# Kernel tuning notes

Measured on AMD Instinct MI355X. Metric: run time of the kernel, lower is better.

The kernel has to match this reference:

```python
import jax, jax.numpy as jnp
import numpy as np

N, D = 16384, 256

def setup_inputs() -> dict:
    key = jax.random.key(0)
    k1, k2 = jax.random.split(key)
    image_features = jax.random.normal(k1, (N, D), dtype=jnp.float32)
    text_features = jax.random.normal(k2, (N, D), dtype=jnp.float32)
    logit_scale = jnp.float32(14.285714)  # exp(log(1/0.07)), typical CLIP temperature
    targets = jnp.arange(N, dtype=jnp.int64)
    return {"image_features": image_features, "text_features": text_features,
            "logit_scale": logit_scale, "targets": targets}

def _cross_entropy(logits, targets):
    # mean over rows of -log_softmax(logits)[i, targets[i]]
    logp = jax.nn.log_softmax(logits, axis=-1)
    return -jnp.mean(jnp.take_along_axis(logp, targets[:, None], axis=-1))

def reference(image_features, text_features, logit_scale, targets):
    logits = logit_scale * (image_features @ text_features.T)  # [N, N]
    image_loss = _cross_entropy(logits, targets)
    text_loss = _cross_entropy(logits.T, targets)
    return (image_loss + text_loss) / 2.0
```

## Files before the change

### kernel.cpp

```cpp
#include <hip/hip_runtime.h>

#define N_ 16384
#define D_ 256
#define LOG2E 1.4426950408889634f
#define HEXP2(x) __builtin_amdgcn_exp2f(x)

typedef __attribute__((ext_vector_type(8))) short short8;
typedef __attribute__((ext_vector_type(16))) float floatx16;

typedef __attribute__((address_space(1))) const unsigned int gu32_t;
typedef __attribute__((address_space(3))) unsigned int lu32_t;

__device__ __forceinline__ void async16(const void* g, void* l) {
  __builtin_amdgcn_global_load_lds((gu32_t*)g, (lu32_t*)l, 16, 0, 0);
}

__device__ __forceinline__ unsigned short f2bf(float x) {
  unsigned int u = __float_as_uint(x);
  u += 0x7fffu + ((u >> 16) & 1u);
  return (unsigned short)(u >> 16);
}

__global__ void prep_pack(const float* __restrict__ img, const float* __restrict__ txt,
                          const float* __restrict__ ls, short* __restrict__ PA,
                          short* __restrict__ PB, float* __restrict__ accv) {
  int t = blockIdx.x * 256 + threadIdx.x;
  int row = t >> 5, kq = t & 31;
  int G = row >> 5, m = row & 31, ks = kq >> 1, h = kq & 1;
  int uidx = (G * 16 + ks) * 64 + h * 32 + m;
  float s2 = ls[0] * LOG2E;
  const float4* sa = (const float4*)(img + (size_t)row * D_ + kq * 8);
  const float4* sb = (const float4*)(txt + (size_t)row * D_ + kq * 8);
  float4 a0 = sa[0], a1 = sa[1];
  float4 b0 = sb[0], b1 = sb[1];
  short8 oa, ob;
  oa[0] = (short)f2bf(a0.x * s2); oa[1] = (short)f2bf(a0.y * s2);
  oa[2] = (short)f2bf(a0.z * s2); oa[3] = (short)f2bf(a0.w * s2);
  oa[4] = (short)f2bf(a1.x * s2); oa[5] = (short)f2bf(a1.y * s2);
  oa[6] = (short)f2bf(a1.z * s2); oa[7] = (short)f2bf(a1.w * s2);
  ob[0] = (short)f2bf(b0.x); ob[1] = (short)f2bf(b0.y);
  ob[2] = (short)f2bf(b0.z); ob[3] = (short)f2bf(b0.w);
  ob[4] = (short)f2bf(b1.x); ob[5] = (short)f2bf(b1.y);
  ob[6] = (short)f2bf(b1.z); ob[7] = (short)f2bf(b1.w);
  ((short8*)PA)[uidx] = oa;
  ((short8*)PB)[uidx] = ob;
  if (t == 0) accv[0] = 0.0f;
}

__global__ void diag_kernel(const float* __restrict__ img, const float* __restrict__ txt,
                            const float* __restrict__ ls, float* __restrict__ diag2) {
  int row = blockIdx.x * 4 + (threadIdx.x >> 6);
  int lane = threadIdx.x & 63;
  float4 a = ((const float4*)(img + (size_t)row * D_))[lane];
  float4 b = ((const float4*)(txt + (size_t)row * D_))[lane];
  float s = a.x * b.x + a.y * b.y + a.z * b.z + a.w * b.w;
  #pragma unroll
  for (int off = 1; off < 64; off <<= 1) s += __shfl_xor(s, off);
  if (lane == 0) diag2[row] = s * ls[0] * LOG2E;
}

__global__ __launch_bounds__(256, 2)
void gemm_stats(const short* __restrict__ PA, const short* __restrict__ PB,
                float2* __restrict__ pR, float2* __restrict__ pC) {
  __shared__ __align__(16) char smem[73728];
  float* rowbuf  = (float*)(smem + 32768);
  float2* colbuf = (float2*)(smem + 71680);

  const int tid = threadIdx.x, lane = tid & 63, wv = tid >> 6;
  const int wr = wv >> 1, wc = wv & 1;
  const int m = lane & 31, h = lane >> 5;
  const int stripe = blockIdx.x, by = blockIdx.y;

  short8 areg[2][16];
  #pragma unroll
  for (int g = 0; g < 2; ++g)
    #pragma unroll
    for (int ks = 0; ks < 16; ++ks)
      areg[g][ks] = *(const short8*)(PA +
          ((size_t)((stripe * 4 + wr * 2 + g) * 16 + ks)) * 512 + lane * 8);
  asm volatile("s_waitcnt vmcnt(0)" ::: "memory");

  floatx16 acc[2][2];

  auto issue = [&](int jj2, int c2, int bufsel) {
    const short* base = PB + ((size_t)((by * 64 + jj2 * 4) * 16) + c2 * 4 + wv) * 512 + lane * 8;
    char* dst = smem + bufsel * 16384 + wv * 1024;
    #pragma unroll
    for (int ct = 0; ct < 4; ++ct)
      async16(base + (size_t)ct * 8192, dst + ct * 4096);
  };
  auto compute = [&](int c, int bufsel) {
    char* base = smem + bufsel * 16384 + lane * 16;
    #pragma unroll
    for (int ksl = 0; ksl < 4; ++ksl) {
      short8 b0 = *(const short8*)(base + ((wc * 2 + 0) * 4 + ksl) * 1024);
      short8 b1 = *(const short8*)(base + ((wc * 2 + 1) * 4 + ksl) * 1024);
      int ks = c * 4 + ksl;
      acc[0][0] = __builtin_amdgcn_mfma_f32_32x32x16_bf16(areg[0][ks], b0, acc[0][0], 0, 0, 0);
      acc[1][0] = __builtin_amdgcn_mfma_f32_32x32x16_bf16(areg[1][ks], b0, acc[1][0], 0, 0, 0);
      acc[0][1] = __builtin_amdgcn_mfma_f32_32x32x16_bf16(areg[0][ks], b1, acc[0][1], 0, 0, 0);
      acc[1][1] = __builtin_amdgcn_mfma_f32_32x32x16_bf16(areg[1][ks], b1, acc[1][1], 0, 0, 0);
    }
  };

  issue(0, 0, 0);
  issue(0, 1, 1);

  float Mr = -3.0e38f, Sr = 0.f;

  for (int jj = 0; jj < 16; ++jj) {
    #pragma unroll
    for (int rt = 0; rt < 2; ++rt)
      #pragma unroll
      for (int ctl = 0; ctl < 2; ++ctl)
        #pragma unroll
        for (int r = 0; r < 16; ++r) acc[rt][ctl][r] = 0.f;

    #pragma unroll
    for (int c = 0; c < 4; ++c) {
      if (jj == 15 && c == 3) { asm volatile("s_waitcnt vmcnt(0)" ::: "memory"); }
      else                    { asm volatile("s_waitcnt vmcnt(4)" ::: "memory"); }
      __builtin_amdgcn_s_barrier();
      asm volatile("" ::: "memory");
      compute(c, c & 1);
      asm volatile("" ::: "memory");
      __builtin_amdgcn_s_barrier();
      asm volatile("" ::: "memory");
      int nc = c + 2;
      int jj2 = jj + (nc >> 2);
      if (jj2 < 16) issue(jj2, nc & 3, nc & 1);
    }

    float v = -3.0e38f;
    #pragma unroll
    for (int rt = 0; rt < 2; ++rt)
      #pragma unroll
      for (int ctl = 0; ctl < 2; ++ctl)
        #pragma unroll
        for (int r = 0; r < 16; ++r) v = fmaxf(v, acc[rt][ctl][r]);
    #pragma unroll
    for (int off = 1; off < 64; off <<= 1) v = fmaxf(v, __shfl_xor(v, off));
    float msub = v - 96.f;

    #pragma unroll
    for (int rt = 0; rt < 2; ++rt)
      #pragma unroll
      for (int ctl = 0; ctl < 2; ++ctl)
        #pragma unroll
        for (int r = 0; r < 16; ++r) acc[rt][ctl][r] = HEXP2(acc[rt][ctl][r] - msub);

    #pragma unroll
    for (int ctl = 0; ctl < 2; ++ctl) {
      float cp = 0.f;
      #pragma unroll
      for (int r = 0; r < 16; ++r) cp += acc[0][ctl][r] + acc[1][ctl][r];
      cp += __shfl_xor(cp, 32);
      if (h == 0) colbuf[wr * 128 + wc * 64 + ctl * 32 + m] = make_float2(msub, cp);
    }

    #pragma unroll
    for (int rt = 0; rt < 2; ++rt)
      #pragma unroll
      for (int rq = 0; rq < 4; ++rq) {
        float4 rp;
        rp.x = acc[rt][0][rq * 4 + 0] + acc[rt][1][rq * 4 + 0];
        rp.y = acc[rt][0][rq * 4 + 1] + acc[rt][1][rq * 4 + 1];
        rp.z = acc[rt][0][rq * 4 + 2] + acc[rt][1][rq * 4 + 2];
        rp.w = acc[rt][0][rq * 4 + 3] + acc[rt][1][rq * 4 + 3];
        *(float4*)&rowbuf[(wr * 64 + wc * 32 + m) * 76 + rt * 32 + rq * 8 + h * 4] = rp;
      }
    asm volatile("s_waitcnt lgkmcnt(0)" ::: "memory");
    __builtin_amdgcn_s_barrier();
    asm volatile("" ::: "memory");

    {
      float s = 0.f;
      #pragma unroll
      for (int k = 0; k < 32; ++k)
        s += rowbuf[(wr * 64 + h * 32 + k) * 76 + wc * 32 + m];
      s += __shfl_xor(s, 32);
      if (s > 0.f) {
        if (msub > Mr) { Sr = Sr * HEXP2(Mr - msub) + s; Mr = msub; }
        else           { Sr += s * HEXP2(msub - Mr); }
      }
    }
    if (tid < 128) {
      float2 c0 = colbuf[tid], c1 = colbuf[128 + tid];
      float M = -3.0e38f, L = 0.f;
      if (c0.y > 0.f) { M = c0.x; L = c0.y; }
      if (c1.y > 0.f) {
        if (c1.x > M) { L = L * HEXP2(M - c1.x) + c1.y; M = c1.x; }
        else          { L += c1.y * HEXP2(c1.x - M); }
      }
      pC[(size_t)stripe * N_ + by * 2048 + jj * 128 + tid] = make_float2(M, L);
    }
    asm volatile("s_waitcnt lgkmcnt(0)" ::: "memory");
    __builtin_amdgcn_s_barrier();
    asm volatile("" ::: "memory");
  }

  if (h == 0)
    pR[(size_t)by * N_ + stripe * 128 + wr * 64 + wc * 32 + m] = make_float2(Mr, Sr);
}

__global__ void merge_kernel(const float2* __restrict__ pR, const float2* __restrict__ pC,
                             const float* __restrict__ diag2, float* __restrict__ accv) {
  int idx = blockIdx.x * 256 + threadIdx.x;
  float M = -3.0e38f, L = 0.f;
  int i;
  if (idx < N_) {
    i = idx;
    #pragma unroll
    for (int g = 0; g < 8; ++g) {
      float2 w = pR[(size_t)g * N_ + i];
      if (w.y > 0.f) {
        if (w.x > M) { L = L * exp2f(M - w.x) + w.y; M = w.x; }
        else         { L += w.y * exp2f(w.x - M); }
      }
    }
  } else {
    i = idx - N_;
    for (int s = 0; s < 128; ++s) {
      float2 w = pC[(size_t)s * N_ + i];
      if (w.y > 0.f) {
        if (w.x > M) { L = L * exp2f(M - w.x) + w.y; M = w.x; }
        else         { L += w.y * exp2f(w.x - M); }
      }
    }
  }
  float val = (M + log2f(fmaxf(L, 1e-45f))) - diag2[i];

  __shared__ float red[256];
  red[threadIdx.x] = val;
  __syncthreads();
  #pragma unroll
  for (int s = 128; s > 0; s >>= 1) {
    if (threadIdx.x < s) red[threadIdx.x] += red[threadIdx.x + s];
    __syncthreads();
  }
  if (threadIdx.x == 0) atomicAdd(accv, red[0]);
}

__global__ void finalize_kernel(const float* __restrict__ accv, float* __restrict__ out) {
  out[0] = accv[0] * (0.69314718055994531f / 32768.0f);
}

extern "C" void kernel_launch(void* const* d_in, const int* in_sizes, int n_in,
                              void* d_out, int out_size, void* d_ws, size_t ws_size,
                              hipStream_t stream) {
  const float* img = (const float*)d_in[0];
  const float* txt = (const float*)d_in[1];
  const float* ls  = (const float*)d_in[2];
  float* out = (float*)d_out;

  char* ws = (char*)d_ws;
  short* PA    = (short*)(ws);
  short* PB    = (short*)(ws + 8388608);
  float* diag2 = (float*)(ws + 16777216);
  float* accv  = (float*)(ws + 16842752);
  float2* pR   = (float2*)(ws + 16843008);
  float2* pC   = (float2*)(ws + 17891584);

  hipLaunchKernelGGL(prep_pack, dim3(2048), dim3(256), 0, stream, img, txt, ls, PA, PB, accv);
  hipLaunchKernelGGL(diag_kernel, dim3(N_ / 4), dim3(256), 0, stream, img, txt, ls, diag2);
  hipLaunchKernelGGL(gemm_stats, dim3(128, 8), dim3(256), 0, stream, PA, PB, pR, pC);
  hipLaunchKernelGGL(merge_kernel, dim3(2 * N_ / 256), dim3(256), 0, stream, pR, pC, diag2, accv);
  hipLaunchKernelGGL(finalize_kernel, dim3(1), dim3(1), 0, stream, accv, out);
}
```

Baseline: 278.5 us.

## Software-pipeline softmax stats behind next tile's MFMAs, fuse diag into pack

The GEMM kernel switches to double-buffered accumulators, so the exp/max/sum statistics of the previous 128x128 tile are computed in four slices interleaved with the MFMA work of the current tile. Each wave now owns 32 rows by 128 columns, which removes the block-wide row-sum exchange and one barrier per tile. The diagonal dot product is fused into the packing kernel, removing a launch and a re-read of the inputs, and the column merge uses four independent accumulator chains for more ILP. The trade-offs are more accumulator registers, which may hurt occupancy at two blocks per CU, and more complex barrier ordering.

```diff
diff --git a/kernel.cpp b/kernel.cpp
--- a/kernel.cpp
+++ b/kernel.cpp
@@ -23,14 +23,16 @@
 
 __global__ void prep_pack(const float* __restrict__ img, const float* __restrict__ txt,
                           const float* __restrict__ ls, short* __restrict__ PA,
-                          short* __restrict__ PB, float* __restrict__ accv) {
-  int t = blockIdx.x * 256 + threadIdx.x;
-  int row = t >> 5, kq = t & 31;
-  int G = row >> 5, m = row & 31, ks = kq >> 1, h = kq & 1;
-  int uidx = (G * 16 + ks) * 64 + h * 32 + m;
-  float s2 = ls[0] * LOG2E;
-  const float4* sa = (const float4*)(img + (size_t)row * D_ + kq * 8);
-  const float4* sb = (const float4*)(txt + (size_t)row * D_ + kq * 8);
+                          short* __restrict__ PB, float* __restrict__ diag2,
+                          float* __restrict__ accv) {
+  const int tid = threadIdx.x;
+  const int t = blockIdx.x * 1024 + tid;
+  const int m = tid & 31, h = (tid >> 5) & 1, ks = (tid >> 6) & 15;
+  const int G = blockIdx.x;
+  const int row = G * 32 + m, col = ks * 16 + h * 8;
+  const float s2 = ls[0] * LOG2E;
+  const float4* sa = (const float4*)(img + (size_t)row * D_ + col);
+  const float4* sb = (const float4*)(txt + (size_t)row * D_ + col);
   float4 a0 = sa[0], a1 = sa[1];
   float4 b0 = sb[0], b1 = sb[1];
   short8 oa, ob;
@@ -42,87 +44,144 @@
   ob[2] = (short)f2bf(b0.z); ob[3] = (short)f2bf(b0.w);
   ob[4] = (short)f2bf(b1.x); ob[5] = (short)f2bf(b1.y);
   ob[6] = (short)f2bf(b1.z); ob[7] = (short)f2bf(b1.w);
-  ((short8*)PA)[uidx] = oa;
-  ((short8*)PB)[uidx] = ob;
-  if (t == 0) accv[0] = 0.0f;
-}
-
-__global__ void diag_kernel(const float* __restrict__ img, const float* __restrict__ txt,
-                            const float* __restrict__ ls, float* __restrict__ diag2) {
-  int row = blockIdx.x * 4 + (threadIdx.x >> 6);
-  int lane = threadIdx.x & 63;
-  float4 a = ((const float4*)(img + (size_t)row * D_))[lane];
-  float4 b = ((const float4*)(txt + (size_t)row * D_))[lane];
-  float s = a.x * b.x + a.y * b.y + a.z * b.z + a.w * b.w;
-  #pragma unroll
-  for (int off = 1; off < 64; off <<= 1) s += __shfl_xor(s, off);
-  if (lane == 0) diag2[row] = s * ls[0] * LOG2E;
+  ((short8*)PA)[t] = oa;
+  ((short8*)PB)[t] = ob;
+
+  float d = a0.x * b0.x + a0.y * b0.y + a0.z * b0.z + a0.w * b0.w
+          + a1.x * b1.x + a1.y * b1.y + a1.z * b1.z + a1.w * b1.w;
+  __shared__ float red[32][33];
+  red[tid >> 5][m] = d;
+  __syncthreads();
+  if (tid < 32) {
+    float s = 0.f;
+    #pragma unroll
+    for (int q = 0; q < 32; ++q) s += red[q][tid];
+    diag2[G * 32 + tid] = s * s2;
+  }
+  if (t == 0) accv[0] = 0.f;
 }
 
 __global__ __launch_bounds__(256, 2)
 void gemm_stats(const short* __restrict__ PA, const short* __restrict__ PB,
                 float2* __restrict__ pR, float2* __restrict__ pC) {
-  __shared__ __align__(16) char smem[73728];
-  float* rowbuf  = (float*)(smem + 32768);
-  float2* colbuf = (float2*)(smem + 71680);
-
-  const int tid = threadIdx.x, lane = tid & 63, wv = tid >> 6;
-  const int wr = wv >> 1, wc = wv & 1;
+  __shared__ __align__(16) char smem[55296];
+  float2* cbuf = (float2*)(smem + 51200);
+
+  const int tid = threadIdx.x, lane = tid & 63, w = tid >> 6;
   const int m = lane & 31, h = lane >> 5;
   const int stripe = blockIdx.x, by = blockIdx.y;
-
-  short8 areg[2][16];
+  float* rbw = (float*)(smem + 32768 + w * 4608);
+
+  short8 areg[16];
   #pragma unroll
-  for (int g = 0; g < 2; ++g)
-    #pragma unroll
-    for (int ks = 0; ks < 16; ++ks)
-      areg[g][ks] = *(const short8*)(PA +
-          ((size_t)((stripe * 4 + wr * 2 + g) * 16 + ks)) * 512 + lane * 8);
+  for (int ks = 0; ks < 16; ++ks)
+    areg[ks] = *(const short8*)(PA + ((size_t)((stripe * 4 + w) * 16 + ks)) * 512 + lane * 8);
   asm volatile("s_waitcnt vmcnt(0)" ::: "memory");
 
-  floatx16 acc[2][2];
+  floatx16 accA[4], accB[4];
+  float Mr = -3.0e38f, Sr = 0.f;
+  float msub = 0.f;
 
   auto issue = [&](int jj2, int c2, int bufsel) {
-    const short* base = PB + ((size_t)((by * 64 + jj2 * 4) * 16) + c2 * 4 + wv) * 512 + lane * 8;
-    char* dst = smem + bufsel * 16384 + wv * 1024;
+    const short* base = PB + ((size_t)((by * 64 + jj2 * 4) * 16) + c2 * 4 + w) * 512 + lane * 8;
+    char* dst = smem + bufsel * 16384 + w * 1024;
     #pragma unroll
     for (int ct = 0; ct < 4; ++ct)
       async16(base + (size_t)ct * 8192, dst + ct * 4096);
   };
-  auto compute = [&](int c, int bufsel) {
+
+  auto compute = [&](int c, int bufsel, floatx16 (&cur)[4]) {
     char* base = smem + bufsel * 16384 + lane * 16;
     #pragma unroll
     for (int ksl = 0; ksl < 4; ++ksl) {
-      short8 b0 = *(const short8*)(base + ((wc * 2 + 0) * 4 + ksl) * 1024);
-      short8 b1 = *(const short8*)(base + ((wc * 2 + 1) * 4 + ksl) * 1024);
-      int ks = c * 4 + ksl;
-      acc[0][0] = __builtin_amdgcn_mfma_f32_32x32x16_bf16(areg[0][ks], b0, acc[0][0], 0, 0, 0);
-      acc[1][0] = __builtin_amdgcn_mfma_f32_32x32x16_bf16(areg[1][ks], b0, acc[1][0], 0, 0, 0);
-      acc[0][1] = __builtin_amdgcn_mfma_f32_32x32x16_bf16(areg[0][ks], b1, acc[0][1], 0, 0, 0);
-      acc[1][1] = __builtin_amdgcn_mfma_f32_32x32x16_bf16(areg[1][ks], b1, acc[1][1], 0, 0, 0);
-    }
-  };
-
-  issue(0, 0, 0);
-  issue(0, 1, 1);
-
-  float Mr = -3.0e38f, Sr = 0.f;
-
-  for (int jj = 0; jj < 16; ++jj) {
-    #pragma unroll
-    for (int rt = 0; rt < 2; ++rt)
+      short8 b0 = *(const short8*)(base + (0 * 4 + ksl) * 1024);
+      short8 b1 = *(const short8*)(base + (1 * 4 + ksl) * 1024);
+      short8 b2 = *(const short8*)(base + (2 * 4 + ksl) * 1024);
+      short8 b3 = *(const short8*)(base + (3 * 4 + ksl) * 1024);
+      const int ks = c * 4 + ksl;
+      cur[0] = __builtin_amdgcn_mfma_f32_32x32x16_bf16(areg[ks], b0, cur[0], 0, 0, 0);
+      cur[1] = __builtin_amdgcn_mfma_f32_32x32x16_bf16(areg[ks], b1, cur[1], 0, 0, 0);
+      cur[2] = __builtin_amdgcn_mfma_f32_32x32x16_bf16(areg[ks], b2, cur[2], 0, 0, 0);
+      cur[3] = __builtin_amdgcn_mfma_f32_32x32x16_bf16(areg[ks], b3, cur[3], 0, 0, 0);
+    }
+  };
+
+  auto stats0 = [&](floatx16 (&pv)[4]) {
+    float mg[4];
+    #pragma unroll
+    for (int g = 0; g < 4; ++g) {
+      float a  = fmaxf(fmaxf(pv[g][0],  pv[g][1]),  fmaxf(pv[g][2],  pv[g][3]));
+      float b  = fmaxf(fmaxf(pv[g][4],  pv[g][5]),  fmaxf(pv[g][6],  pv[g][7]));
+      float c2 = fmaxf(fmaxf(pv[g][8],  pv[g][9]),  fmaxf(pv[g][10], pv[g][11]));
+      float d  = fmaxf(fmaxf(pv[g][12], pv[g][13]), fmaxf(pv[g][14], pv[g][15]));
+      mg[g] = fmaxf(fmaxf(a, b), fmaxf(c2, d));
+    }
+    float v = fmaxf(fmaxf(mg[0], mg[1]), fmaxf(mg[2], mg[3]));
+    #pragma unroll
+    for (int off = 1; off < 64; off <<= 1) v = fmaxf(v, __shfl_xor(v, off));
+    msub = v - 96.f;
+    #pragma unroll
+    for (int g = 0; g < 2; ++g)
       #pragma unroll
-      for (int ctl = 0; ctl < 2; ++ctl)
-        #pragma unroll
-        for (int r = 0; r < 16; ++r) acc[rt][ctl][r] = 0.f;
-
+      for (int r = 0; r < 16; ++r) pv[g][r] = HEXP2(pv[g][r] - msub);
+  };
+  auto stats1 = [&](floatx16 (&pv)[4]) {
+    #pragma unroll
+    for (int g = 2; g < 4; ++g)
+      #pragma unroll
+      for (int r = 0; r < 16; ++r) pv[g][r] = HEXP2(pv[g][r] - msub);
+  };
+  auto stats2 = [&](floatx16 (&pv)[4]) {
+    #pragma unroll
+    for (int r = 0; r < 16; ++r) {
+      float s = (pv[0][r] + pv[1][r]) + (pv[2][r] + pv[3][r]);
+      rbw[((r & 3) + 8 * (r >> 2) + 4 * h) * 36 + m] = s;
+    }
+  };
+  auto stats3 = [&](floatx16 (&pv)[4]) {
+    asm volatile("s_waitcnt lgkmcnt(0)" ::: "memory");
+    const float* src = rbw + m * 36 + h * 16;
+    float4 q0 = *(const float4*)(src + 0);
+    float4 q1 = *(const float4*)(src + 4);
+    float4 q2 = *(const float4*)(src + 8);
+    float4 q3 = *(const float4*)(src + 12);
+    float s = ((q0.x + q0.y) + (q0.z + q0.w)) + ((q1.x + q1.y) + (q1.z + q1.w))
+            + ((q2.x + q2.y) + (q2.z + q2.w)) + ((q3.x + q3.y) + (q3.z + q3.w));
+    s += __shfl_xor(s, 32);
+    if (s > 0.f) {
+      if (msub > Mr) { Sr = Sr * HEXP2(Mr - msub) + s; Mr = msub; }
+      else           { Sr += s * HEXP2(msub - Mr); }
+    }
+    #pragma unroll
+    for (int g = 0; g < 4; ++g) {
+      float cp = ((pv[g][0]  + pv[g][1])  + (pv[g][2]  + pv[g][3]))
+               + ((pv[g][4]  + pv[g][5])  + (pv[g][6]  + pv[g][7]))
+               + ((pv[g][8]  + pv[g][9])  + (pv[g][10] + pv[g][11]))
+               + ((pv[g][12] + pv[g][13]) + (pv[g][14] + pv[g][15]));
+      cp += __shfl_xor(cp, 32);
+      if (h == 0) cbuf[w * 128 + g * 32 + m] = make_float2(msub, cp);
+    }
+  };
+
+  auto tile = [&](int jj, floatx16 (&cur)[4], floatx16 (&prev)[4],
+                  bool do_stats, int jc, bool last) {
+    #pragma unroll
+    for (int g = 0; g < 4; ++g)
+      #pragma unroll
+      for (int r = 0; r < 16; ++r) cur[g][r] = 0.f;
     #pragma unroll
     for (int c = 0; c < 4; ++c) {
-      if (jj == 15 && c == 3) { asm volatile("s_waitcnt vmcnt(0)" ::: "memory"); }
-      else                    { asm volatile("s_waitcnt vmcnt(4)" ::: "memory"); }
+      if (last && c == 3) { asm volatile("s_waitcnt vmcnt(0)" ::: "memory"); }
+      else                { asm volatile("s_waitcnt vmcnt(4)" ::: "memory"); }
       __builtin_amdgcn_s_barrier();
       asm volatile("" ::: "memory");
-      compute(c, c & 1);
+      compute(c, c & 1, cur);
+      if (do_stats) {
+        if (c == 0)      stats0(prev);
+        else if (c == 1) stats1(prev);
+        else if (c == 2) stats2(prev);
+        else             stats3(prev);
+      }
       asm volatile("" ::: "memory");
       __builtin_amdgcn_s_barrier();
       asm volatile("" ::: "memory");
@@ -130,103 +189,77 @@
       int jj2 = jj + (nc >> 2);
       if (jj2 < 16) issue(jj2, nc & 3, nc & 1);
     }
-
-    float v = -3.0e38f;
-    #pragma unroll
-    for (int rt = 0; rt < 2; ++rt)
+    if (do_stats && tid < 128) {
+      float M = -3.0e38f, L = 0.f;
       #pragma unroll
-      for (int ctl = 0; ctl < 2; ++ctl)
-        #pragma unroll
-        for (int r = 0; r < 16; ++r) v = fmaxf(v, acc[rt][ctl][r]);
-    #pragma unroll
-    for (int off = 1; off < 64; off <<= 1) v = fmaxf(v, __shfl_xor(v, off));
-    float msub = v - 96.f;
-
-    #pragma unroll
-    for (int rt = 0; rt < 2; ++rt)
-      #pragma unroll
-      for (int ctl = 0; ctl < 2; ++ctl)
-        #pragma unroll
-        for (int r = 0; r < 16; ++r) acc[rt][ctl][r] = HEXP2(acc[rt][ctl][r] - msub);
-
-    #pragma unroll
-    for (int ctl = 0; ctl < 2; ++ctl) {
-      float cp = 0.f;
-      #pragma unroll
-      for (int r = 0; r < 16; ++r) cp += acc[0][ctl][r] + acc[1][ctl][r];
-      cp += __shfl_xor(cp, 32);
-      if (h == 0) colbuf[wr * 128 + wc * 64 + ctl * 32 + m] = make_float2(msub, cp);
-    }
-
-    #pragma unroll
-    for (int rt = 0; rt < 2; ++rt)
-      #pragma unroll
-      for (int rq = 0; rq < 4; ++rq) {
-        float4 rp;
-        rp.x = acc[rt][0][rq * 4 + 0] + acc[rt][1][rq * 4 + 0];
-        rp.y = acc[rt][0][rq * 4 + 1] + acc[rt][1][rq * 4 + 1];
-        rp.z = acc[rt][0][rq * 4 + 2] + acc[rt][1][rq * 4 + 2];
-        rp.w = acc[rt][0][rq * 4 + 3] + acc[rt][1][rq * 4 + 3];
-        *(float4*)&rowbuf[(wr * 64 + wc * 32 + m) * 76 + rt * 32 + rq * 8 + h * 4] = rp;
+      for (int s4 = 0; s4 < 4; ++s4) {
+        float2 pp = cbuf[s4 * 128 + tid];
+        if (pp.y > 0.f) {
+          if (pp.x > M) { L = L * HEXP2(M - pp.x) + pp.y; M = pp.x; }
+          else          { L += pp.y * HEXP2(pp.x - M); }
+        }
       }
-    asm volatile("s_waitcnt lgkmcnt(0)" ::: "memory");
-    __builtin_amdgcn_s_barrier();
-    asm volatile("" ::: "memory");
-
-    {
-      float s = 0.f;
-      #pragma unroll
-      for (int k = 0; k < 32; ++k)
-        s += rowbuf[(wr * 64 + h * 32 + k) * 76 + wc * 32 + m];
-      s += __shfl_xor(s, 32);
-      if (s > 0.f) {
-        if (msub > Mr) { Sr = Sr * HEXP2(Mr - msub) + s; Mr = msub; }
-        else           { Sr += s * HEXP2(msub - Mr); }
+      pC[(size_t)stripe * N_ + by * 2048 + jc * 128 + tid] = make_float2(M, L);
+    }
+  };
+
+  issue(0, 0, 0);
+  issue(0, 1, 1);
+
+  tile(0, accA, accB, false, 0, false);
+  #pragma unroll 1
+  for (int p = 0; p < 7; ++p) {
+    tile(2 * p + 1, accB, accA, true, 2 * p,     false);
+    tile(2 * p + 2, accA, accB, true, 2 * p + 1, false);
+  }
+  tile(15, accB, accA, true, 14, true);
+
+  stats0(accB); stats1(accB); stats2(accB); stats3(accB);
+  __syncthreads();
+  if (tid < 128) {
+    float M = -3.0e38f, L = 0.f;
+    #pragma unroll
+    for (int s4 = 0; s4 < 4; ++s4) {
+      float2 pp = cbuf[s4 * 128 + tid];
+      if (pp.y > 0.f) {
+        if (pp.x > M) { L = L * HEXP2(M - pp.x) + pp.y; M = pp.x; }
+        else          { L += pp.y * HEXP2(pp.x - M); }
       }
     }
-    if (tid < 128) {
-      float2 c0 = colbuf[tid], c1 = colbuf[128 + tid];
-      float M = -3.0e38f, L = 0.f;
-      if (c0.y > 0.f) { M = c0.x; L = c0.y; }
-      if (c1.y > 0.f) {
-        if (c1.x > M) { L = L * HEXP2(M - c1.x) + c1.y; M = c1.x; }
-        else          { L += c1.y * HEXP2(c1.x - M); }
-      }
-      pC[(size_t)stripe * N_ + by * 2048 + jj * 128 + tid] = make_float2(M, L);
-    }
-    asm volatile("s_waitcnt lgkmcnt(0)" ::: "memory");
-    __builtin_amdgcn_s_barrier();
-    asm volatile("" ::: "memory");
-  }
-
-  if (h == 0)
-    pR[(size_t)by * N_ + stripe * 128 + wr * 64 + wc * 32 + m] = make_float2(Mr, Sr);
+    pC[(size_t)stripe * N_ + by * 2048 + 15 * 128 + tid] = make_float2(M, L);
+  }
+  if (lane < 32)
+    pR[(size_t)by * N_ + stripe * 128 + w * 32 + lane] = make_float2(Mr, Sr);
 }
 
 __global__ void merge_kernel(const float2* __restrict__ pR, const float2* __restrict__ pC,
                              const float* __restrict__ diag2, float* __restrict__ accv) {
+  auto mrg = [](float& M, float& L, float2 w) {
+    if (w.y > 0.f) {
+      if (w.x > M) { L = L * exp2f(M - w.x) + w.y; M = w.x; }
+      else         { L += w.y * exp2f(w.x - M); }
+    }
+  };
   int idx = blockIdx.x * 256 + threadIdx.x;
   float M = -3.0e38f, L = 0.f;
   int i;
   if (idx < N_) {
     i = idx;
     #pragma unroll
-    for (int g = 0; g < 8; ++g) {
-      float2 w = pR[(size_t)g * N_ + i];
-      if (w.y > 0.f) {
-        if (w.x > M) { L = L * exp2f(M - w.x) + w.y; M = w.x; }
-        else         { L += w.y * exp2f(w.x - M); }
-      }
-    }
+    for (int g = 0; g < 8; ++g) mrg(M, L, pR[(size_t)g * N_ + i]);
   } else {
     i = idx - N_;
-    for (int s = 0; s < 128; ++s) {
-      float2 w = pC[(size_t)s * N_ + i];
-      if (w.y > 0.f) {
-        if (w.x > M) { L = L * exp2f(M - w.x) + w.y; M = w.x; }
-        else         { L += w.y * exp2f(w.x - M); }
-      }
-    }
+    float M1 = -3.0e38f, L1 = 0.f, M2 = -3.0e38f, L2 = 0.f, M3 = -3.0e38f, L3 = 0.f;
+    #pragma unroll 4
+    for (int s = 0; s < 128; s += 4) {
+      mrg(M,  L,  pC[(size_t)(s + 0) * N_ + i]);
+      mrg(M1, L1, pC[(size_t)(s + 1) * N_ + i]);
+      mrg(M2, L2, pC[(size_t)(s + 2) * N_ + i]);
+      mrg(M3, L3, pC[(size_t)(s + 3) * N_ + i]);
+    }
+    mrg(M, L, make_float2(M1, L1));
+    mrg(M, L, make_float2(M2, L2));
+    mrg(M, L, make_float2(M3, L3));
   }
   float val = (M + log2f(fmaxf(L, 1e-45f))) - diag2[i];
 
@@ -261,8 +294,7 @@
   float2* pR   = (float2*)(ws + 16843008);
   float2* pC   = (float2*)(ws + 17891584);
 
-  hipLaunchKernelGGL(prep_pack, dim3(2048), dim3(256), 0, stream, img, txt, ls, PA, PB, accv);
-  hipLaunchKernelGGL(diag_kernel, dim3(N_ / 4), dim3(256), 0, stream, img, txt, ls, diag2);
+  hipLaunchKernelGGL(prep_pack, dim3(512), dim3(1024), 0, stream, img, txt, ls, PA, PB, diag2, accv);
   hipLaunchKernelGGL(gemm_stats, dim3(128, 8), dim3(256), 0, stream, PA, PB, pR, pC);
   hipLaunchKernelGGL(merge_kernel, dim3(2 * N_ / 256), dim3(256), 0, stream, pR, pC, diag2, accv);
   hipLaunchKernelGGL(finalize_kernel, dim3(1), dim3(1), 0, stream, accv, out);
```

Measured after the change: 299.8 us. +7.6%, slower.

## Fuse diag into pack kernel, drop finalize, tree max, setprio, split merge chains

Applied to the files above, without the earlier changes.

The diagonal dot-product kernel is folded into the bf16 pack kernel, which now handles one 32-row group per 1024-thread block and reduces the diagonal through shared memory. The finalize kernel is removed by scaling inside the merge kernel's atomicAdd into the output, cutting two launches and one reread of the inputs. The GEMM wraps its MFMA burst in s_setprio, and the row-max becomes a tree reduction for more instruction-level parallelism. The column merge uses four independent online-softmax chains to hide load and exp latency. Zeroing the output in the pack kernel depends on kernel ordering on the stream.

```diff
diff --git a/kernel.cpp b/kernel.cpp
--- a/kernel.cpp
+++ b/kernel.cpp
@@ -23,14 +23,16 @@
 
 __global__ void prep_pack(const float* __restrict__ img, const float* __restrict__ txt,
                           const float* __restrict__ ls, short* __restrict__ PA,
-                          short* __restrict__ PB, float* __restrict__ accv) {
-  int t = blockIdx.x * 256 + threadIdx.x;
-  int row = t >> 5, kq = t & 31;
-  int G = row >> 5, m = row & 31, ks = kq >> 1, h = kq & 1;
-  int uidx = (G * 16 + ks) * 64 + h * 32 + m;
-  float s2 = ls[0] * LOG2E;
-  const float4* sa = (const float4*)(img + (size_t)row * D_ + kq * 8);
-  const float4* sb = (const float4*)(txt + (size_t)row * D_ + kq * 8);
+                          short* __restrict__ PB, float* __restrict__ diag2,
+                          float* __restrict__ out) {
+  const int tid = threadIdx.x;
+  const int t = blockIdx.x * 1024 + tid;
+  const int m = tid & 31, h = (tid >> 5) & 1, ks = (tid >> 6) & 15;
+  const int G = blockIdx.x;
+  const int row = G * 32 + m, col = ks * 16 + h * 8;
+  const float s2 = ls[0] * LOG2E;
+  const float4* sa = (const float4*)(img + (size_t)row * D_ + col);
+  const float4* sb = (const float4*)(txt + (size_t)row * D_ + col);
   float4 a0 = sa[0], a1 = sa[1];
   float4 b0 = sb[0], b1 = sb[1];
   short8 oa, ob;
@@ -42,21 +44,21 @@
   ob[2] = (short)f2bf(b0.z); ob[3] = (short)f2bf(b0.w);
   ob[4] = (short)f2bf(b1.x); ob[5] = (short)f2bf(b1.y);
   ob[6] = (short)f2bf(b1.z); ob[7] = (short)f2bf(b1.w);
-  ((short8*)PA)[uidx] = oa;
-  ((short8*)PB)[uidx] = ob;
-  if (t == 0) accv[0] = 0.0f;
-}
-
-__global__ void diag_kernel(const float* __restrict__ img, const float* __restrict__ txt,
-                            const float* __restrict__ ls, float* __restrict__ diag2) {
-  int row = blockIdx.x * 4 + (threadIdx.x >> 6);
-  int lane = threadIdx.x & 63;
-  float4 a = ((const float4*)(img + (size_t)row * D_))[lane];
-  float4 b = ((const float4*)(txt + (size_t)row * D_))[lane];
-  float s = a.x * b.x + a.y * b.y + a.z * b.z + a.w * b.w;
-  #pragma unroll
-  for (int off = 1; off < 64; off <<= 1) s += __shfl_xor(s, off);
-  if (lane == 0) diag2[row] = s * ls[0] * LOG2E;
+  ((short8*)PA)[t] = oa;
+  ((short8*)PB)[t] = ob;
+
+  float d = a0.x * b0.x + a0.y * b0.y + a0.z * b0.z + a0.w * b0.w
+          + a1.x * b1.x + a1.y * b1.y + a1.z * b1.z + a1.w * b1.w;
+  __shared__ float red[32][33];
+  red[tid >> 5][m] = d;
+  __syncthreads();
+  if (tid < 32) {
+    float s = 0.f;
+    #pragma unroll
+    for (int q = 0; q < 32; ++q) s += red[q][tid];
+    diag2[G * 32 + tid] = s * s2;
+  }
+  if (t == 0) out[0] = 0.f;
 }
 
 __global__ __launch_bounds__(256, 2)
@@ -91,6 +93,7 @@
   };
   auto compute = [&](int c, int bufsel) {
     char* base = smem + bufsel * 16384 + lane * 16;
+    __builtin_amdgcn_s_setprio(1);
     #pragma unroll
     for (int ksl = 0; ksl < 4; ++ksl) {
       short8 b0 = *(const short8*)(base + ((wc * 2 + 0) * 4 + ksl) * 1024);
@@ -101,6 +104,7 @@
       acc[0][1] = __builtin_amdgcn_mfma_f32_32x32x16_bf16(areg[0][ks], b1, acc[0][1], 0, 0, 0);
       acc[1][1] = __builtin_amdgcn_mfma_f32_32x32x16_bf16(areg[1][ks], b1, acc[1][1], 0, 0, 0);
     }
+    __builtin_amdgcn_s_setprio(0);
   };
 
   issue(0, 0, 0);
@@ -131,13 +135,21 @@
       if (jj2 < 16) issue(jj2, nc & 3, nc & 1);
     }
 
-    float v = -3.0e38f;
-    #pragma unroll
-    for (int rt = 0; rt < 2; ++rt)
-      #pragma unroll
-      for (int ctl = 0; ctl < 2; ++ctl)
-        #pragma unroll
-        for (int r = 0; r < 16; ++r) v = fmaxf(v, acc[rt][ctl][r]);
+    float vm[4];
+    #pragma unroll
+    for (int q = 0; q < 4; ++q) {
+      float a01 = fmaxf(acc[q >> 1][q & 1][0],  acc[q >> 1][q & 1][1]);
+      float a23 = fmaxf(acc[q >> 1][q & 1][2],  acc[q >> 1][q & 1][3]);
+      float a45 = fmaxf(acc[q >> 1][q & 1][4],  acc[q >> 1][q & 1][5]);
+      float a67 = fmaxf(acc[q >> 1][q & 1][6],  acc[q >> 1][q & 1][7]);
+      float a89 = fmaxf(acc[q >> 1][q & 1][8],  acc[q >> 1][q & 1][9]);
+      float aab = fmaxf(acc[q >> 1][q & 1][10], acc[q >> 1][q & 1][11]);
+      float acd = fmaxf(acc[q >> 1][q & 1][12], acc[q >> 1][q & 1][13]);
+      float aef = fmaxf(acc[q >> 1][q & 1][14], acc[q >> 1][q & 1][15]);
+      vm[q] = fmaxf(fmaxf(fmaxf(a01, a23), fmaxf(a45, a67)),
+                    fmaxf(fmaxf(a89, aab), fmaxf(acd, aef)));
+    }
+    float v = fmaxf(fmaxf(vm[0], vm[1]), fmaxf(vm[2], vm[3]));
     #pragma unroll
     for (int off = 1; off < 64; off <<= 1) v = fmaxf(v, __shfl_xor(v, off));
     float msub = v - 96.f;
@@ -204,29 +216,33 @@
 }
 
 __global__ void merge_kernel(const float2* __restrict__ pR, const float2* __restrict__ pC,
-                             const float* __restrict__ diag2, float* __restrict__ accv) {
+                             const float* __restrict__ diag2, float* __restrict__ out) {
+  auto mrg = [](float& M, float& L, float2 w) {
+    if (w.y > 0.f) {
+      if (w.x > M) { L = L * exp2f(M - w.x) + w.y; M = w.x; }
+      else         { L += w.y * exp2f(w.x - M); }
+    }
+  };
   int idx = blockIdx.x * 256 + threadIdx.x;
   float M = -3.0e38f, L = 0.f;
   int i;
   if (idx < N_) {
     i = idx;
     #pragma unroll
-    for (int g = 0; g < 8; ++g) {
-      float2 w = pR[(size_t)g * N_ + i];
-      if (w.y > 0.f) {
-        if (w.x > M) { L = L * exp2f(M - w.x) + w.y; M = w.x; }
-        else         { L += w.y * exp2f(w.x - M); }
-      }
-    }
+    for (int g = 0; g < 8; ++g) mrg(M, L, pR[(size_t)g * N_ + i]);
   } else {
     i = idx - N_;
-    for (int s = 0; s < 128; ++s) {
-      float2 w = pC[(size_t)s * N_ + i];
-      if (w.y > 0.f) {
-        if (w.x > M) { L = L * exp2f(M - w.x) + w.y; M = w.x; }
-        else         { L += w.y * exp2f(w.x - M); }
-      }
-    }
+    float M1 = -3.0e38f, L1 = 0.f, M2 = -3.0e38f, L2 = 0.f, M3 = -3.0e38f, L3 = 0.f;
+    #pragma unroll 4
+    for (int s = 0; s < 128; s += 4) {
+      mrg(M,  L,  pC[(size_t)(s + 0) * N_ + i]);
+      mrg(M1, L1, pC[(size_t)(s + 1) * N_ + i]);
+      mrg(M2, L2, pC[(size_t)(s + 2) * N_ + i]);
+      mrg(M3, L3, pC[(size_t)(s + 3) * N_ + i]);
+    }
+    mrg(M, L, make_float2(M1, L1));
+    mrg(M, L, make_float2(M2, L2));
+    mrg(M, L, make_float2(M3, L3));
   }
   float val = (M + log2f(fmaxf(L, 1e-45f))) - diag2[i];
 
@@ -238,11 +254,8 @@
     if (threadIdx.x < s) red[threadIdx.x] += red[threadIdx.x + s];
     __syncthreads();
   }
-  if (threadIdx.x == 0) atomicAdd(accv, red[0]);
-}
-
-__global__ void finalize_kernel(const float* __restrict__ accv, float* __restrict__ out) {
-  out[0] = accv[0] * (0.69314718055994531f / 32768.0f);
+  if (threadIdx.x == 0)
+    atomicAdd(out, red[0] * (0.69314718055994531f / 32768.0f));
 }
 
 extern "C" void kernel_launch(void* const* d_in, const int* in_sizes, int n_in,
@@ -257,13 +270,10 @@
   short* PA    = (short*)(ws);
   short* PB    = (short*)(ws + 8388608);
   float* diag2 = (float*)(ws + 16777216);
-  float* accv  = (float*)(ws + 16842752);
   float2* pR   = (float2*)(ws + 16843008);
   float2* pC   = (float2*)(ws + 17891584);
 
-  hipLaunchKernelGGL(prep_pack, dim3(2048), dim3(256), 0, stream, img, txt, ls, PA, PB, accv);
-  hipLaunchKernelGGL(diag_kernel, dim3(N_ / 4), dim3(256), 0, stream, img, txt, ls, diag2);
+  hipLaunchKernelGGL(prep_pack, dim3(512), dim3(1024), 0, stream, img, txt, ls, PA, PB, diag2, out);
   hipLaunchKernelGGL(gemm_stats, dim3(128, 8), dim3(256), 0, stream, PA, PB, pR, pC);
-  hipLaunchKernelGGL(merge_kernel, dim3(2 * N_ / 256), dim3(256), 0, stream, pR, pC, diag2, accv);
-  hipLaunchKernelGGL(finalize_kernel, dim3(1), dim3(1), 0, stream, accv, out);
-}
+  hipLaunchKernelGGL(merge_kernel, dim3(2 * N_ / 256), dim3(256), 0, stream, pR, pC, diag2, out);
+}
```

Measured after the change: 282.1 us. No clear change (+1.3%).
